# Optimization experiments

Measured on AMD Instinct MI355X. Metric: run time of the kernel, lower is better.

Reference implementation:

```python
import jax, jax.numpy as jnp
import numpy as np

EPS = 1e-7  # K.epsilon()


def setup_inputs() -> dict:
    key = jax.random.key(0)
    k1, k2, k3 = jax.random.split(key, 3)
    B, H, W, Cin, Cout, KH, KW = 8, 128, 128, 256, 256, 3, 3
    x = jax.random.normal(k1, (B, H, W, Cin), dtype=jnp.float32)
    style = jax.random.normal(k2, (B, Cin), dtype=jnp.float32)
    # he_uniform-ish scale for the kernel
    fan_in = KH * KW * Cin
    limit = np.sqrt(6.0 / fan_in)
    kernel = jax.random.uniform(k3, (KH, KW, Cin, Cout), dtype=jnp.float32,
                                minval=-limit, maxval=limit)
    return {"x": x, "style": style, "kernel": kernel}


def reference(x, style, kernel):
    # Demodulation factor: rsqrt(sum_{kh,kw,cin} (kernel * style)^2 + eps), shape (B, Cout).
    # Equivalent to the original's broadcast-then-reduce, computed without
    # materializing the (B,kh,kw,Cin,Cout) modulated weight tensor.
    k2 = jnp.sum(jnp.square(kernel), axis=(0, 1))          # (Cin, Cout)
    ssq = jnp.einsum('io,bi->bo', k2, jnp.square(style))   # (B, Cout)
    demod = jax.lax.rsqrt(ssq + EPS)                       # (B, Cout)

    # Modulate input per-sample, then shared-weight conv (same padding, stride 1).
    xm = x * style[:, None, None, :]                       # (B,H,W,Cin)
    y = jax.lax.conv_general_dilated(
        xm, kernel,
        window_strides=(1, 1), padding='SAME',
        dimension_numbers=('NHWC', 'HWIO', 'NHWC'))
    return y * demod[:, None, None, :]
```

## Files before the change

### kernel.cpp

```cpp
#include <hip/hip_runtime.h>
#include <hip/hip_bf16.h>
#include <stdint.h>

typedef short short8 __attribute__((ext_vector_type(8)));
typedef float f32x4 __attribute__((ext_vector_type(4)));

#define PXS 40

__device__ __forceinline__ short f2bf(float f) {
    __hip_bfloat16 h = __float2bfloat16(f);
    return __builtin_bit_cast(short, h);
}

__global__ void prep_k2(const float* __restrict__ kern, float* __restrict__ K2)
{
    const int ci = blockIdx.x, co = threadIdx.x;
    float acc = 0.f;
#pragma unroll
    for (int p = 0; p < 9; ++p) {
        float w = kern[(p * 256 + ci) * 256 + co];
        acc += w * w;
    }
    K2[ci * 256 + co] = acc;
}

__global__ void prep_demod(const float* __restrict__ style,
                           const float* __restrict__ K2,
                           float* __restrict__ demod)
{
    const int b = blockIdx.x, co = threadIdx.x;
    __shared__ float s2[256];
    float s = style[b * 256 + co];
    s2[co] = s * s;
    __syncthreads();
    float acc = 0.f;
#pragma unroll 8
    for (int ci = 0; ci < 256; ++ci)
        acc += s2[ci] * K2[ci * 256 + co];
    demod[b * 256 + co] = 1.0f / sqrtf(acc + 1e-7f);
}

__global__ void prep_kf(const float* __restrict__ kern,
                        __hip_bfloat16* __restrict__ kf)
{
    const int st = blockIdx.x;
    const int sl = st / 3, tp = st - sl * 3;
    const int dh = sl >> 3, cc = sl & 7;
    const int p  = dh * 3 + tp;
    const int t    = threadIdx.x;
    const int lane = t & 63, jt2 = t >> 6;
    const int l15  = lane & 15, lk = lane >> 4;
    const int cib  = cc * 32 + lk * 8;
#pragma unroll
    for (int jj = 0; jj < 4; ++jj) {
        const int jt = jj * 4 + jt2;
        const int co = jt * 16 + l15;
        short8 v;
#pragma unroll
        for (int e = 0; e < 8; ++e)
            v[e] = f2bf(kern[(size_t)(p * 256 + cib + e) * 256 + co]);
        *(short8*)(kf + ((size_t)(st * 16 + jt) * 64 + lane) * 8) = v;
    }
}

__global__ __launch_bounds__(256) void conv_mfma(
    const float* __restrict__ x,
    const __hip_bfloat16* __restrict__ kf,
    const float* __restrict__ style,
    const float* __restrict__ demod,
    float* __restrict__ out)
{
    __shared__ __align__(16) __hip_bfloat16 Xs[2][130 * PXS];
    __shared__ __align__(16) __hip_bfloat16 KfB[2][24 * 512];
    __shared__ float Ss[256];
    __shared__ float Ds[128];

    const int t    = threadIdx.x;
    const int bid  = blockIdx.x;
    const int L    = ((bid & 7) << 8) | (bid >> 3);
    const int n0   = (L & 1) << 7;
    const int bh   = L >> 1;
    const int b    = bh >> 7, h = bh & 127;
    const int wave = t >> 6, lane = t & 63;
    const int wr   = (wave >> 1) << 6;
    const int wc   = (wave & 1) << 6;
    const int wjl  = (wave & 1) << 2;
    const int l15  = lane & 15, lk = lane >> 4;
    const int mA   = t >> 2;
    const int koff = (t & 3) << 3;
    const int jb0  = (L & 1) << 3;

    if (t < 128) {
        ((float2*)Ss)[t] = ((const float2*)(style + b * 256))[t];
        Ds[t] = demod[b * 256 + n0 + t];
    }
    if (t < 32) {
        const __hip_bfloat16 z = __float2bfloat16(0.f);
        Xs[0][t] = z; Xs[0][129 * PXS + t] = z;
        Xs[1][t] = z; Xs[1][129 * PXS + t] = z;
    }

    f32x4 acc[4][4] = {};

    const int slo = (h == 0)   ? 8  : 0;
    const int shi = (h == 127) ? 16 : 24;

    auto stage_kf = [&](int s, int buf) {
#pragma unroll
        for (int k = 0; k < 6; ++k) {
            const int c = (k << 2) + wave;
            const __hip_bfloat16* src =
                kf + ((size_t)(s * 48 + ((c >> 3) << 4) + jb0 + (c & 7)) * 64
                      + lane) * 8;
            __builtin_amdgcn_global_load_lds(
                (const __attribute__((address_space(1))) void*)src,
                (__attribute__((address_space(3))) void*)&KfB[buf][c * 512],
                16, 0, 0);
        }
    };

    __syncthreads();

    stage_kf(slo, 0);
    {
        const int h2  = h + (slo >> 3) - 1;
        const int ci0 = (slo & 7) << 5;
        const size_t rowbase = (size_t)(b * 128 + h2) * 128;
        const float* ga = x + (rowbase + mA)      * 256 + ci0 + koff;
        const float* gb = x + (rowbase + mA + 64) * 256 + ci0 + koff;
        float4 xa0 = *(const float4*)ga, xa1 = *(const float4*)(ga + 4);
        float4 xb0 = *(const float4*)gb, xb1 = *(const float4*)(gb + 4);
        float4 s0  = *(const float4*)&Ss[ci0 + koff];
        float4 s1  = *(const float4*)&Ss[ci0 + koff + 4];
        short8 ma, mb;
#pragma unroll
        for (int jj = 0; jj < 4; ++jj) {
            ma[jj]     = f2bf((&xa0.x)[jj] * (&s0.x)[jj]);
            ma[jj + 4] = f2bf((&xa1.x)[jj] * (&s1.x)[jj]);
            mb[jj]     = f2bf((&xb0.x)[jj] * (&s0.x)[jj]);
            mb[jj + 4] = f2bf((&xb1.x)[jj] * (&s1.x)[jj]);
        }
        *(short8*)&Xs[0][(mA + 1)  * PXS + koff] = ma;
        *(short8*)&Xs[0][(mA + 65) * PXS + koff] = mb;
    }
    __syncthreads();

    int cur = 0;
    for (int s = slo; s < shi; ++s, cur ^= 1) {
        const bool pf = (s + 1 < shi);
        float4 xa0, xa1, xb0, xb1;
        int nci0 = 0;
        if (pf) {
            const int sl = s + 1;
            const int h2 = h + (sl >> 3) - 1;
            nci0 = (sl & 7) << 5;
            const size_t rowbase = (size_t)(b * 128 + h2) * 128;
            const float* ga = x + (rowbase + mA)      * 256 + nci0 + koff;
            const float* gb = x + (rowbase + mA + 64) * 256 + nci0 + koff;
            xa0 = *(const float4*)ga; xa1 = *(const float4*)(ga + 4);
            xb0 = *(const float4*)gb; xb1 = *(const float4*)(gb + 4);
            stage_kf(sl, cur ^ 1);
        }

#pragma unroll
        for (int tp = 0; tp < 3; ++tp) {
            short8 af[4], bfr[4];
#pragma unroll
            for (int j = 0; j < 4; ++j)
                bfr[j] = *(const short8*)&KfB[cur][((tp << 3) + wjl + j) * 512
                                                   + lane * 8];
#pragma unroll
            for (int i = 0; i < 4; ++i)
                af[i] = *(const short8*)&Xs[cur][(wr + i * 16 + l15 + tp) * PXS
                                                 + lk * 8];
#pragma unroll
            for (int i = 0; i < 4; ++i)
#pragma unroll
                for (int j = 0; j < 4; ++j)
                    acc[i][j] = __builtin_amdgcn_mfma_f32_16x16x32_bf16(
                        af[i], bfr[j], acc[i][j], 0, 0, 0);
        }

        if (pf) {
            float4 s0 = *(const float4*)&Ss[nci0 + koff];
            float4 s1 = *(const float4*)&Ss[nci0 + koff + 4];
            short8 ma, mb;
#pragma unroll
            for (int jj = 0; jj < 4; ++jj) {
                ma[jj]     = f2bf((&xa0.x)[jj] * (&s0.x)[jj]);
                ma[jj + 4] = f2bf((&xa1.x)[jj] * (&s1.x)[jj]);
                mb[jj]     = f2bf((&xb0.x)[jj] * (&s0.x)[jj]);
                mb[jj + 4] = f2bf((&xb1.x)[jj] * (&s1.x)[jj]);
            }
            *(short8*)&Xs[cur ^ 1][(mA + 1)  * PXS + koff] = ma;
            *(short8*)&Xs[cur ^ 1][(mA + 65) * PXS + koff] = mb;
        }
        __syncthreads();
    }

    float dj[4];
#pragma unroll
    for (int j = 0; j < 4; ++j) dj[j] = Ds[wc + j * 16 + l15];
    const size_t obase = (size_t)(b * 128 + h) * 128 * 256 + n0;
#pragma unroll
    for (int i = 0; i < 4; ++i) {
#pragma unroll
        for (int j = 0; j < 4; ++j) {
            const int n = wc + j * 16 + l15;
#pragma unroll
            for (int r = 0; r < 4; ++r) {
                const int m = wr + i * 16 + lk * 4 + r;
                out[obase + (size_t)m * 256 + n] = acc[i][j][r] * dj[j];
            }
        }
    }
}

extern "C" void kernel_launch(void* const* d_in, const int* in_sizes, int n_in,
                              void* d_out, int out_size, void* d_ws, size_t ws_size,
                              hipStream_t stream)
{
    const float* x     = (const float*)d_in[0];
    const float* style = (const float*)d_in[1];
    const float* kern  = (const float*)d_in[2];
    float* out = (float*)d_out;

    char*  ws    = (char*)d_ws;
    float* demod = (float*)ws;
    float* K2    = (float*)(ws + 8192);
    __hip_bfloat16* kT = (__hip_bfloat16*)(ws + 270336);

    prep_k2   <<<256, 256, 0, stream>>>(kern, K2);
    prep_demod<<<8,   256, 0, stream>>>(style, K2, demod);
    prep_kf   <<<72,  256, 0, stream>>>(kern, kT);
    conv_mfma <<<2048, 256, 0, stream>>>(x, kT, style, demod, out);
}
```

Measured before the change: 367.4 us.

## Precompute bf16 modulated input and stage it via async LDS loads with swizzle

```diff
diff --git a/kernel.cpp b/kernel.cpp
--- a/kernel.cpp
+++ b/kernel.cpp
@@ -5,11 +5,29 @@
 typedef short short8 __attribute__((ext_vector_type(8)));
 typedef float f32x4 __attribute__((ext_vector_type(4)));
 
-#define PXS 40
-
 __device__ __forceinline__ short f2bf(float f) {
     __hip_bfloat16 h = __float2bfloat16(f);
     return __builtin_bit_cast(short, h);
+}
+
+__global__ void prep_xm(const float* __restrict__ x,
+                        const float* __restrict__ style,
+                        __hip_bfloat16* __restrict__ xm)
+{
+    const size_t gi = ((size_t)blockIdx.x * 256 + threadIdx.x) * 8;
+    const int b  = (int)(gi >> 22);
+    const int ci = (int)(gi & 255);
+    float4 x0 = *(const float4*)(x + gi);
+    float4 x1 = *(const float4*)(x + gi + 4);
+    float4 s0 = *(const float4*)(style + b * 256 + ci);
+    float4 s1 = *(const float4*)(style + b * 256 + ci + 4);
+    short8 m;
+#pragma unroll
+    for (int jj = 0; jj < 4; ++jj) {
+        m[jj]     = f2bf((&x0.x)[jj] * (&s0.x)[jj]);
+        m[jj + 4] = f2bf((&x1.x)[jj] * (&s1.x)[jj]);
+    }
+    *(short8*)(xm + gi) = m;
 }
 
 __global__ void prep_k2(const float* __restrict__ kern, float* __restrict__ K2)
@@ -64,15 +82,13 @@
 }
 
 __global__ __launch_bounds__(256) void conv_mfma(
-    const float* __restrict__ x,
+    const __hip_bfloat16* __restrict__ xm,
     const __hip_bfloat16* __restrict__ kf,
-    const float* __restrict__ style,
     const float* __restrict__ demod,
     float* __restrict__ out)
 {
-    __shared__ __align__(16) __hip_bfloat16 Xs[2][130 * PXS];
+    __shared__ __align__(16) __hip_bfloat16 Xs[2][130 * 32];
     __shared__ __align__(16) __hip_bfloat16 KfB[2][24 * 512];
-    __shared__ float Ss[256];
     __shared__ float Ds[128];
 
     const int t    = threadIdx.x;
@@ -86,18 +102,13 @@
     const int wc   = (wave & 1) << 6;
     const int wjl  = (wave & 1) << 2;
     const int l15  = lane & 15, lk = lane >> 4;
-    const int mA   = t >> 2;
-    const int koff = (t & 3) << 3;
     const int jb0  = (L & 1) << 3;
 
-    if (t < 128) {
-        ((float2*)Ss)[t] = ((const float2*)(style + b * 256))[t];
-        Ds[t] = demod[b * 256 + n0 + t];
-    }
+    if (t < 128) Ds[t] = demod[b * 256 + n0 + t];
     if (t < 32) {
         const __hip_bfloat16 z = __float2bfloat16(0.f);
-        Xs[0][t] = z; Xs[0][129 * PXS + t] = z;
-        Xs[1][t] = z; Xs[1][129 * PXS + t] = z;
+        Xs[0][t] = z; Xs[0][129 * 32 + t] = z;
+        Xs[1][t] = z; Xs[1][129 * 32 + t] = z;
     }
 
     f32x4 acc[4][4] = {};
@@ -105,7 +116,25 @@
     const int slo = (h == 0)   ? 8  : 0;
     const int shi = (h == 127) ? 16 : 24;
 
-    auto stage_kf = [&](int s, int buf) {
+    auto stage_A = [&](int s, int buf) {
+        const int h2  = h + (s >> 3) - 1;
+        const int ci0 = (s & 7) << 5;
+        const size_t rowbase = (size_t)(b * 128 + h2) * 128;
+        const int lr = lane >> 2, slot = lane & 3;
+#pragma unroll
+        for (int k = 0; k < 2; ++k) {
+            const int d = (wave << 1) | k;
+            const int r = 1 + (d << 4) + lr;
+            const int c = slot ^ ((r >> 1) & 3);
+            const __hip_bfloat16* src =
+                xm + (rowbase + (r - 1)) * 256 + ci0 + (c << 3);
+            __builtin_amdgcn_global_load_lds(
+                (const __attribute__((address_space(1))) void*)src,
+                (__attribute__((address_space(3))) void*)&Xs[buf][(1 + (d << 4)) * 32],
+                16, 0, 0);
+        }
+    };
+    auto stage_B = [&](int s, int buf) {
 #pragma unroll
         for (int k = 0; k < 6; ++k) {
             const int c = (k << 2) + wave;
@@ -119,47 +148,15 @@
         }
     };
 
-    __syncthreads();
-
-    stage_kf(slo, 0);
-    {
-        const int h2  = h + (slo >> 3) - 1;
-        const int ci0 = (slo & 7) << 5;
-        const size_t rowbase = (size_t)(b * 128 + h2) * 128;
-        const float* ga = x + (rowbase + mA)      * 256 + ci0 + koff;
-        const float* gb = x + (rowbase + mA + 64) * 256 + ci0 + koff;
-        float4 xa0 = *(const float4*)ga, xa1 = *(const float4*)(ga + 4);
-        float4 xb0 = *(const float4*)gb, xb1 = *(const float4*)(gb + 4);
-        float4 s0  = *(const float4*)&Ss[ci0 + koff];
-        float4 s1  = *(const float4*)&Ss[ci0 + koff + 4];
-        short8 ma, mb;
-#pragma unroll
-        for (int jj = 0; jj < 4; ++jj) {
-            ma[jj]     = f2bf((&xa0.x)[jj] * (&s0.x)[jj]);
-            ma[jj + 4] = f2bf((&xa1.x)[jj] * (&s1.x)[jj]);
-            mb[jj]     = f2bf((&xb0.x)[jj] * (&s0.x)[jj]);
-            mb[jj + 4] = f2bf((&xb1.x)[jj] * (&s1.x)[jj]);
-        }
-        *(short8*)&Xs[0][(mA + 1)  * PXS + koff] = ma;
-        *(short8*)&Xs[0][(mA + 65) * PXS + koff] = mb;
-    }
+    stage_A(slo, 0);
+    stage_B(slo, 0);
     __syncthreads();
 
     int cur = 0;
     for (int s = slo; s < shi; ++s, cur ^= 1) {
-        const bool pf = (s + 1 < shi);
-        float4 xa0, xa1, xb0, xb1;
-        int nci0 = 0;
-        if (pf) {
-            const int sl = s + 1;
-            const int h2 = h + (sl >> 3) - 1;
-            nci0 = (sl & 7) << 5;
-            const size_t rowbase = (size_t)(b * 128 + h2) * 128;
-            const float* ga = x + (rowbase + mA)      * 256 + nci0 + koff;
-            const float* gb = x + (rowbase + mA + 64) * 256 + nci0 + koff;
-            xa0 = *(const float4*)ga; xa1 = *(const float4*)(ga + 4);
-            xb0 = *(const float4*)gb; xb1 = *(const float4*)(gb + 4);
-            stage_kf(sl, cur ^ 1);
+        if (s + 1 < shi) {
+            stage_A(s + 1, cur ^ 1);
+            stage_B(s + 1, cur ^ 1);
         }
 
 #pragma unroll
@@ -170,9 +167,11 @@
                 bfr[j] = *(const short8*)&KfB[cur][((tp << 3) + wjl + j) * 512
                                                    + lane * 8];
 #pragma unroll
-            for (int i = 0; i < 4; ++i)
-                af[i] = *(const short8*)&Xs[cur][(wr + i * 16 + l15 + tp) * PXS
-                                                 + lk * 8];
+            for (int i = 0; i < 4; ++i) {
+                const int R = wr + i * 16 + l15 + tp;
+                af[i] = *(const short8*)&Xs[cur][R * 32
+                                                 + ((lk ^ ((R >> 1) & 3)) << 3)];
+            }
 #pragma unroll
             for (int i = 0; i < 4; ++i)
 #pragma unroll
@@ -180,21 +179,6 @@
                     acc[i][j] = __builtin_amdgcn_mfma_f32_16x16x32_bf16(
                         af[i], bfr[j], acc[i][j], 0, 0, 0);
         }
-
-        if (pf) {
-            float4 s0 = *(const float4*)&Ss[nci0 + koff];
-            float4 s1 = *(const float4*)&Ss[nci0 + koff + 4];
-            short8 ma, mb;
-#pragma unroll
-            for (int jj = 0; jj < 4; ++jj) {
-                ma[jj]     = f2bf((&xa0.x)[jj] * (&s0.x)[jj]);
-                ma[jj + 4] = f2bf((&xa1.x)[jj] * (&s1.x)[jj]);
-                mb[jj]     = f2bf((&xb0.x)[jj] * (&s0.x)[jj]);
-                mb[jj + 4] = f2bf((&xb1.x)[jj] * (&s1.x)[jj]);
-            }
-            *(short8*)&Xs[cur ^ 1][(mA + 1)  * PXS + koff] = ma;
-            *(short8*)&Xs[cur ^ 1][(mA + 65) * PXS + koff] = mb;
-        }
         __syncthreads();
     }
 
@@ -209,7 +193,7 @@
             const int n = wc + j * 16 + l15;
 #pragma unroll
             for (int r = 0; r < 4; ++r) {
-                const int m = wr + i * 16 + lk * 4 + r;
+                const int m = wr + i * 16 + (lane >> 4) * 4 + r;
                 out[obase + (size_t)m * 256 + n] = acc[i][j][r] * dj[j];
             }
         }
@@ -225,13 +209,15 @@
     const float* kern  = (const float*)d_in[2];
     float* out = (float*)d_out;
 
-    char*  ws    = (char*)d_ws;
-    float* demod = (float*)ws;
-    float* K2    = (float*)(ws + 8192);
-    __hip_bfloat16* kT = (__hip_bfloat16*)(ws + 270336);
-
-    prep_k2   <<<256, 256, 0, stream>>>(kern, K2);
-    prep_demod<<<8,   256, 0, stream>>>(style, K2, demod);
-    prep_kf   <<<72,  256, 0, stream>>>(kern, kT);
-    conv_mfma <<<2048, 256, 0, stream>>>(x, kT, style, demod, out);
-}
+    char* ws = (char*)d_ws;
+    __hip_bfloat16* xm = (__hip_bfloat16*)ws;
+    float* demod = (float*)(ws + 67108864);
+    float* K2    = (float*)(ws + 67108864 + 8192);
+    __hip_bfloat16* kT = (__hip_bfloat16*)(ws + 67108864 + 270336);
+
+    prep_xm   <<<16384, 256, 0, stream>>>(x, style, xm);
+    prep_k2   <<<256,   256, 0, stream>>>(kern, K2);
+    prep_demod<<<8,     256, 0, stream>>>(style, K2, demod);
+    prep_kf   <<<72,    256, 0, stream>>>(kern, kT);
+    conv_mfma <<<2048,  256, 0, stream>>>(xm, kT, demod, out);
+}
```

Result: no change. 370.9 us (+0.9%).
